# Optimization experiments

Measured on AMD Instinct MI355X. Metric: run time of the kernel, lower is better.

Reference implementation:

```python
import jax, jax.numpy as jnp
import numpy as np

C = 128          # num_channels
S = 3000         # sequence_num
INTER = 30
EXTRACT = S // INTER  # 100
EPS = 1e-5


def _layernorm(y, g, b):
    # LayerNorm over last (channel) axis, eps=1e-5 like torch default
    m = jnp.mean(y, axis=-1, keepdims=True)
    v = jnp.mean(jnp.square(y - m), axis=-1, keepdims=True)
    return (y - m) * jax.lax.rsqrt(v + EPS) * g + b


def setup_inputs() -> dict:
    key = jax.random.key(0)
    ks = jax.random.split(key, 4)
    x = jax.random.normal(ks[0], (32, 4, C, S), dtype=jnp.float32)
    # xavier_normal Linear weights, zero bias; LayerNorm gamma=1, beta=0
    std = float(np.sqrt(2.0 / (C + C)))
    def lin_w(k):
        return jax.random.normal(k, (C, C), dtype=jnp.float32) * std
    Wq = lin_w(ks[1]); Wk = lin_w(ks[2]); Wp = lin_w(ks[3])
    z = jnp.zeros((C,), jnp.float32); o = jnp.ones((C,), jnp.float32)
    return {
        "x": x,
        "Wq": Wq, "bq": z, "gq": o, "betaq": z,
        "Wk": Wk, "bk": z, "gk": o, "betak": z,
        "Wp": Wp, "bp": z, "gp": o, "betap": z,
    }


def reference(x, Wq, bq, gq, betaq, Wk, bk, gk, betak, Wp, bp, gp, betap):
    # x: [b, o, c, s]
    temp = jnp.swapaxes(x, -1, -2)                         # [b,o,s,c]
    q = _layernorm(temp @ Wq.T + bq, gq, betaq)            # [b,o,s,c]
    k = _layernorm(temp @ Wk.T + bk, gk, betak)            # [b,o,s,c]
    q = jnp.swapaxes(q, -1, -2)                            # [b,o,c,s]
    k = jnp.swapaxes(k, -1, -2)                            # [b,o,c,s]
    scaling = jnp.asarray(EXTRACT, x.dtype) ** 0.5         # sqrt(extract_sequence)
    atten = jnp.einsum('bocs,boms->bocm', q, k) / scaling  # [b,o,c,c]
    score = jax.nn.softmax(atten, axis=-1)                 # [b,o,c,c]
    # faithful to source: contracts m (score rows sum to 1)
    out = jnp.einsum('bocs,bocm->bocs', x, score)          # [b,o,c,s]
    out = jnp.swapaxes(out, -1, -2)                        # [b,o,s,c]
    out = _layernorm(out @ Wp.T + bp, gp, betap)
    return jnp.swapaxes(out, -1, -2)                       # [b,o,c,s]
```

## Files before the change

kernel.cpp:

```cpp
#include <hip/hip_runtime.h>


#define C    128
#define SEQ  3000
#define NG   128
#define NT   128
#define NBLK ((SEQ + NT - 1) / NT)

typedef float f4 __attribute__((ext_vector_type(4)));
typedef short short8 __attribute__((ext_vector_type(8)));

__device__ __forceinline__ unsigned short f2bf(float f) {
    union { float f; unsigned u; } v; v.f = f;
    unsigned r = v.u + 0x7fffu + ((v.u >> 16) & 1u);
    return (unsigned short)(r >> 16);
}

__device__ __forceinline__ unsigned cvt2(float lo, float hi) {
    unsigned r;
    asm("v_cvt_pk_bf16_f32 %0, %1, %2" : "=v"(r) : "v"(lo), "v"(hi));
    return r;
}

__device__ __forceinline__ int swz(int row, int chunk) {
    return chunk ^ ((row ^ (row >> 2)) & 15);
}

__global__ void cvt_wp(const float* __restrict__ Wp, unsigned short* __restrict__ out) {
    int i = blockIdx.x * 256 + threadIdx.x;
    if (i >= C * C) return;
    int c = i >> 7, r = i & 127, ch = r >> 3, j = r & 7;
    out[c * C + swz(c, ch) * 8 + j] = f2bf(Wp[i]);
}

__global__ __launch_bounds__(512, 4) void gemm_ln_mfma(
    const float* __restrict__ x,
    const unsigned short* __restrict__ wbf,
    const float* __restrict__ bp,
    const float* __restrict__ gp,
    const float* __restrict__ bep,
    float* __restrict__ out)
{
    __shared__ __align__(16) unsigned short Wl[C * C];
    __shared__ __align__(16) unsigned short Xl[NT * C];

    const int g  = blockIdx.y;
    const int s0 = blockIdx.x * NT;
    const float* xg = x + (size_t)g * (C * SEQ);
    float* og = out + (size_t)g * (C * SEQ);
    const int t = threadIdx.x;

    {
        const uint4* wsrc = (const uint4*)wbf;
        uint4* wdst = (uint4*)Wl;
        #pragma unroll
        for (int i = 0; i < 4; ++i) wdst[t + 512 * i] = wsrc[t + 512 * i];
    }

    {
        const int sq  = t & 31;
        const int mc  = t >> 5;
        const int s_loc  = 4 * sq;
        const int s_glob = s0 + s_loc;
        const bool valid = (s_glob + 3) < SEQ;
        f4 r[8];
        const float* xp = xg + (size_t)(mc * 8) * SEQ + s_glob;
        #pragma unroll
        for (int rr = 0; rr < 8; ++rr) {
            if (valid) r[rr] = *(const f4*)(xp + (size_t)rr * SEQ);
            else       r[rr] = (f4){0.f, 0.f, 0.f, 0.f};
        }
        #pragma unroll
        for (int j = 0; j < 4; ++j) {
            const int sl = s_loc + j;
            uint4 pk;
            pk.x = cvt2(r[0][j], r[1][j]);
            pk.y = cvt2(r[2][j], r[3][j]);
            pk.z = cvt2(r[4][j], r[5][j]);
            pk.w = cvt2(r[6][j], r[7][j]);
            *(uint4*)&Xl[sl * C + swz(sl, mc) * 8] = pk;
        }
    }
    __syncthreads();

    const int w    = t >> 6;
    const int lane = t & 63;
    const int col  = lane & 15;
    const int quad = lane >> 4;

    f4 acc[8];
    #pragma unroll
    for (int mt = 0; mt < 8; ++mt) acc[mt] = (f4){0.f, 0.f, 0.f, 0.f};

    const int srow = 16 * w + col;

    #pragma unroll 1
    for (int kc = 0; kc < 4; ++kc) {
        short8 xb = *(const short8*)&Xl[srow * C + swz(srow, 4 * kc + quad) * 8];
        short8 a[8];
        #pragma unroll
        for (int mt = 0; mt < 8; ++mt) {
            const int row = 16 * mt + col;
            a[mt] = *(const short8*)&Wl[row * C + swz(row, 4 * kc + quad) * 8];
        }
        #pragma unroll
        for (int mt = 0; mt < 8; ++mt)
            acc[mt] = __builtin_amdgcn_mfma_f32_16x16x32_bf16(a[mt], xb, acc[mt], 0, 0, 0);
    }

    #pragma unroll
    for (int mt = 0; mt < 8; ++mt) {
        const f4 b4 = *(const f4*)(bp + 16 * mt + 4 * quad);
        #pragma unroll
        for (int r = 0; r < 4; ++r) acc[mt][r] += b4[r];
    }

    float s = 0.f, q = 0.f;
    #pragma unroll
    for (int mt = 0; mt < 8; ++mt)
        #pragma unroll
        for (int r = 0; r < 4; ++r) {
            float y = acc[mt][r];
            s += y; q += y * y;
        }
    s += __shfl_xor(s, 16); q += __shfl_xor(q, 16);
    s += __shfl_xor(s, 32); q += __shfl_xor(q, 32);
    const float mean = s * (1.0f / C);
    const float var  = q * (1.0f / C) - mean * mean;
    const float rstd = rsqrtf(var + 1e-5f);

    const int sg = s0 + srow;
    if (sg < SEQ) {
        #pragma unroll
        for (int mt = 0; mt < 8; ++mt) {
            const f4 g4 = *(const f4*)(gp  + 16 * mt + 4 * quad);
            const f4 e4 = *(const f4*)(bep + 16 * mt + 4 * quad);
            #pragma unroll
            for (int r = 0; r < 4; ++r) {
                const int c = 16 * mt + 4 * quad + r;
                og[(size_t)c * SEQ + sg] =
                    (acc[mt][r] - mean) * rstd * g4[r] + e4[r];
            }
        }
    }
}

extern "C" void kernel_launch(void* const* d_in, const int* in_sizes, int n_in,
                              void* d_out, int out_size, void* d_ws, size_t ws_size,
                              hipStream_t stream) {
    const float* x   = (const float*)d_in[0];
    const float* Wp  = (const float*)d_in[9];
    const float* bp  = (const float*)d_in[10];
    const float* gp  = (const float*)d_in[11];
    const float* bep = (const float*)d_in[12];
    float* out = (float*)d_out;
    unsigned short* wbf = (unsigned short*)d_ws;

    hipLaunchKernelGGL(cvt_wp, dim3(64), dim3(256), 0, stream, Wp, wbf);

    dim3 grid(NBLK, NG);
    hipLaunchKernelGGL(gemm_ln_mfma, grid, dim3(512), 0, stream,
                       x, wbf, bp, gp, bep, out);
}
```

Baseline: 374.1 us.

## Make GEMM+LayerNorm blocks loop over six sequence tiles with register prefetch

Each block now handles six consecutive 128-column sequence tiles instead of one, so the grid shrinks to 4x128 blocks. The bf16 weight tile is staged into LDS once per block rather than once per tile. The next tile's x values are loaded into registers while the current tile is converted, stored to LDS and run through MFMA and LayerNorm, hiding global-load latency. Out-of-range loads are clamped rather than zero-filled, and explicit s_barrier/lgkmcnt waits replace __syncthreads. The cost is fewer, longer-running blocks, less parallelism across the GPU and more register pressure.

```diff
diff --git a/kernel.cpp b/kernel.cpp
--- a/kernel.cpp
+++ b/kernel.cpp
@@ -5,7 +5,8 @@
 #define SEQ  3000
 #define NG   128
 #define NT   128
-#define NBLK ((SEQ + NT - 1) / NT)
+#define NTILES 6
+#define NBX  4
 
 typedef float f4 __attribute__((ext_vector_type(4)));
 typedef short short8 __attribute__((ext_vector_type(8)));
@@ -24,6 +25,13 @@
 
 __device__ __forceinline__ int swz(int row, int chunk) {
     return chunk ^ ((row ^ (row >> 2)) & 15);
+}
+
+__device__ __forceinline__ void bar_lgkm() {
+    asm volatile("s_waitcnt lgkmcnt(0)\n\ts_barrier" ::: "memory");
+}
+__device__ __forceinline__ void bar_raw() {
+    asm volatile("s_barrier" ::: "memory");
 }
 
 __global__ void cvt_wp(const float* __restrict__ Wp, unsigned short* __restrict__ out) {
@@ -45,7 +53,7 @@
     __shared__ __align__(16) unsigned short Xl[NT * C];
 
     const int g  = blockIdx.y;
-    const int s0 = blockIdx.x * NT;
+    const int bx = blockIdx.x;
     const float* xg = x + (size_t)g * (C * SEQ);
     float* og = out + (size_t)g * (C * SEQ);
     const int t = threadIdx.x;
@@ -57,91 +65,111 @@
         for (int i = 0; i < 4; ++i) wdst[t + 512 * i] = wsrc[t + 512 * i];
     }
 
-    {
-        const int sq  = t & 31;
-        const int mc  = t >> 5;
-        const int s_loc  = 4 * sq;
-        const int s_glob = s0 + s_loc;
-        const bool valid = (s_glob + 3) < SEQ;
-        f4 r[8];
-        const float* xp = xg + (size_t)(mc * 8) * SEQ + s_glob;
-        #pragma unroll
-        for (int rr = 0; rr < 8; ++rr) {
-            if (valid) r[rr] = *(const f4*)(xp + (size_t)rr * SEQ);
-            else       r[rr] = (f4){0.f, 0.f, 0.f, 0.f};
-        }
-        #pragma unroll
-        for (int j = 0; j < 4; ++j) {
-            const int sl = s_loc + j;
-            uint4 pk;
-            pk.x = cvt2(r[0][j], r[1][j]);
-            pk.y = cvt2(r[2][j], r[3][j]);
-            pk.z = cvt2(r[4][j], r[5][j]);
-            pk.w = cvt2(r[6][j], r[7][j]);
-            *(uint4*)&Xl[sl * C + swz(sl, mc) * 8] = pk;
-        }
-    }
-    __syncthreads();
+    const int sq  = t & 31;
+    const int mc  = t >> 5;
+    const int s_loc = 4 * sq;
 
     const int w    = t >> 6;
     const int lane = t & 63;
     const int col  = lane & 15;
     const int quad = lane >> 4;
-
-    f4 acc[8];
-    #pragma unroll
-    for (int mt = 0; mt < 8; ++mt) acc[mt] = (f4){0.f, 0.f, 0.f, 0.f};
-
     const int srow = 16 * w + col;
 
+    const int s_base = bx * (NTILES * NT);
+
+    f4 r[8];
+    {
+        int sgl = s_base + s_loc;
+        int sc  = sgl > (SEQ - 4) ? (SEQ - 4) : sgl;
+        const float* xp = xg + (size_t)(mc * 8) * SEQ + sc;
+        #pragma unroll
+        for (int rr = 0; rr < 8; ++rr) r[rr] = *(const f4*)(xp + (size_t)rr * SEQ);
+    }
+
     #pragma unroll 1
-    for (int kc = 0; kc < 4; ++kc) {
-        short8 xb = *(const short8*)&Xl[srow * C + swz(srow, 4 * kc + quad) * 8];
-        short8 a[8];
+    for (int tt = 0; tt < NTILES; ++tt) {
+        const int s0 = s_base + tt * NT;
+
+        uint4 pk[4];
+        #pragma unroll
+        for (int j = 0; j < 4; ++j) {
+            pk[j].x = cvt2(r[0][j], r[1][j]);
+            pk[j].y = cvt2(r[2][j], r[3][j]);
+            pk[j].z = cvt2(r[4][j], r[5][j]);
+            pk[j].w = cvt2(r[6][j], r[7][j]);
+        }
+
+        if (tt + 1 < NTILES) {
+            int sgl = s0 + NT + s_loc;
+            int sc  = sgl > (SEQ - 4) ? (SEQ - 4) : sgl;
+            const float* xp = xg + (size_t)(mc * 8) * SEQ + sc;
+            #pragma unroll
+            for (int rr = 0; rr < 8; ++rr) r[rr] = *(const f4*)(xp + (size_t)rr * SEQ);
+        }
+
+        #pragma unroll
+        for (int j = 0; j < 4; ++j) {
+            const int sl = s_loc + j;
+            *(uint4*)&Xl[sl * C + swz(sl, mc) * 8] = pk[j];
+        }
+
+        bar_lgkm();
+
+        f4 acc[8];
+        #pragma unroll
+        for (int mt = 0; mt < 8; ++mt) acc[mt] = (f4){0.f, 0.f, 0.f, 0.f};
+
+        #pragma unroll 1
+        for (int kc = 0; kc < 4; ++kc) {
+            short8 xb = *(const short8*)&Xl[srow * C + swz(srow, 4 * kc + quad) * 8];
+            short8 a[8];
+            #pragma unroll
+            for (int mt = 0; mt < 8; ++mt) {
+                const int row = 16 * mt + col;
+                a[mt] = *(const short8*)&Wl[row * C + swz(row, 4 * kc + quad) * 8];
+            }
+            #pragma unroll
+            for (int mt = 0; mt < 8; ++mt)
+                acc[mt] = __builtin_amdgcn_mfma_f32_16x16x32_bf16(a[mt], xb, acc[mt], 0, 0, 0);
+        }
+
         #pragma unroll
         for (int mt = 0; mt < 8; ++mt) {
-            const int row = 16 * mt + col;
-            a[mt] = *(const short8*)&Wl[row * C + swz(row, 4 * kc + quad) * 8];
+            const f4 b4 = *(const f4*)(bp + 16 * mt + 4 * quad);
+            #pragma unroll
+            for (int rr = 0; rr < 4; ++rr) acc[mt][rr] += b4[rr];
         }
+
+        float s = 0.f, q = 0.f;
         #pragma unroll
         for (int mt = 0; mt < 8; ++mt)
-            acc[mt] = __builtin_amdgcn_mfma_f32_16x16x32_bf16(a[mt], xb, acc[mt], 0, 0, 0);
-    }
+            #pragma unroll
+            for (int rr = 0; rr < 4; ++rr) {
+                float y = acc[mt][rr];
+                s += y; q += y * y;
+            }
+        s += __shfl_xor(s, 16); q += __shfl_xor(q, 16);
+        s += __shfl_xor(s, 32); q += __shfl_xor(q, 32);
+        const float mean = s * (1.0f / C);
+        const float var  = q * (1.0f / C) - mean * mean;
+        const float rstd = rsqrtf(var + 1e-5f);
 
-    #pragma unroll
-    for (int mt = 0; mt < 8; ++mt) {
-        const f4 b4 = *(const f4*)(bp + 16 * mt + 4 * quad);
-        #pragma unroll
-        for (int r = 0; r < 4; ++r) acc[mt][r] += b4[r];
-    }
-
-    float s = 0.f, q = 0.f;
-    #pragma unroll
-    for (int mt = 0; mt < 8; ++mt)
-        #pragma unroll
-        for (int r = 0; r < 4; ++r) {
-            float y = acc[mt][r];
-            s += y; q += y * y;
-        }
-    s += __shfl_xor(s, 16); q += __shfl_xor(q, 16);
-    s += __shfl_xor(s, 32); q += __shfl_xor(q, 32);
-    const float mean = s * (1.0f / C);
-    const float var  = q * (1.0f / C) - mean * mean;
-    const float rstd = rsqrtf(var + 1e-5f);
-
-    const int sg = s0 + srow;
-    if (sg < SEQ) {
-        #pragma unroll
-        for (int mt = 0; mt < 8; ++mt) {
-            const f4 g4 = *(const f4*)(gp  + 16 * mt + 4 * quad);
-            const f4 e4 = *(const f4*)(bep + 16 * mt + 4 * quad);
+        const int sg = s0 + srow;
+        if (sg < SEQ) {
             #pragma unroll
-            for (int r = 0; r < 4; ++r) {
-                const int c = 16 * mt + 4 * quad + r;
-                og[(size_t)c * SEQ + sg] =
-                    (acc[mt][r] - mean) * rstd * g4[r] + e4[r];
+            for (int mt = 0; mt < 8; ++mt) {
+                const f4 g4 = *(const f4*)(gp  + 16 * mt + 4 * quad);
+                const f4 e4 = *(const f4*)(bep + 16 * mt + 4 * quad);
+                #pragma unroll
+                for (int rr = 0; rr < 4; ++rr) {
+                    const int c = 16 * mt + 4 * quad + rr;
+                    og[(size_t)c * SEQ + sg] =
+                        (acc[mt][rr] - mean) * rstd * g4[rr] + e4[rr];
+                }
             }
         }
+
+        bar_raw();
     }
 }
 
@@ -158,7 +186,7 @@
 
     hipLaunchKernelGGL(cvt_wp, dim3(64), dim3(256), 0, stream, Wp, wbf);
 
-    dim3 grid(NBLK, NG);
+    dim3 grid(NBX, NG);
     hipLaunchKernelGGL(gemm_ln_mfma, grid, dim3(512), 0, stream,
                        x, wbf, bp, gp, bep, out);
 }
```

Result: slower. 400.0 us (+6.9%).

## Convert GEMM+LayerNorm to persistent waves with register-prefetched 16-row strips

Applied to the files above, without the earlier changes.

Replaces the one-block-per-128-row-tile grid with a persistent grid of 512 blocks. Each wave independently loops over 16-sequence strips, with a per-wave LDS staging buffer. The next strip's x values are prefetched into registers while the current strip runs its MFMA and LayerNorm, so global load latency overlaps compute. The weight LDS fill and the bias, gamma and beta loads are paid once per block instead of once per tile. The cost is higher register pressure and smaller 16-row MFMA tiles per wave, and the last strip clamps its load address rather than zero-filling.

```diff
diff --git a/kernel.cpp b/kernel.cpp
--- a/kernel.cpp
+++ b/kernel.cpp
@@ -4,8 +4,9 @@
 #define C    128
 #define SEQ  3000
 #define NG   128
-#define NT   128
-#define NBLK ((SEQ + NT - 1) / NT)
+#define SPG  188
+#define NSTRIP (NG * SPG)
+#define NWAVE  4096
 
 typedef float f4 __attribute__((ext_vector_type(4)));
 typedef short short8 __attribute__((ext_vector_type(8)));
@@ -42,12 +43,8 @@
     float* __restrict__ out)
 {
     __shared__ __align__(16) unsigned short Wl[C * C];
-    __shared__ __align__(16) unsigned short Xl[NT * C];
+    __shared__ __align__(16) unsigned short Xs[8][16 * C];
 
-    const int g  = blockIdx.y;
-    const int s0 = blockIdx.x * NT;
-    const float* xg = x + (size_t)g * (C * SEQ);
-    float* og = out + (size_t)g * (C * SEQ);
     const int t = threadIdx.x;
 
     {
@@ -56,90 +53,111 @@
         #pragma unroll
         for (int i = 0; i < 4; ++i) wdst[t + 512 * i] = wsrc[t + 512 * i];
     }
-
-    {
-        const int sq  = t & 31;
-        const int mc  = t >> 5;
-        const int s_loc  = 4 * sq;
-        const int s_glob = s0 + s_loc;
-        const bool valid = (s_glob + 3) < SEQ;
-        f4 r[8];
-        const float* xp = xg + (size_t)(mc * 8) * SEQ + s_glob;
-        #pragma unroll
-        for (int rr = 0; rr < 8; ++rr) {
-            if (valid) r[rr] = *(const f4*)(xp + (size_t)rr * SEQ);
-            else       r[rr] = (f4){0.f, 0.f, 0.f, 0.f};
-        }
-        #pragma unroll
-        for (int j = 0; j < 4; ++j) {
-            const int sl = s_loc + j;
-            uint4 pk;
-            pk.x = cvt2(r[0][j], r[1][j]);
-            pk.y = cvt2(r[2][j], r[3][j]);
-            pk.z = cvt2(r[4][j], r[5][j]);
-            pk.w = cvt2(r[6][j], r[7][j]);
-            *(uint4*)&Xl[sl * C + swz(sl, mc) * 8] = pk;
-        }
-    }
     __syncthreads();
 
     const int w    = t >> 6;
     const int lane = t & 63;
     const int col  = lane & 15;
     const int quad = lane >> 4;
+    const int mc   = lane >> 2;
+    const int sq   = lane & 3;
+    unsigned short* X = &Xs[w][0];
 
-    f4 acc[8];
+    const int wgid = blockIdx.x * 8 + w;
+
+    f4 b4[8], g4[8], e4[8];
     #pragma unroll
-    for (int mt = 0; mt < 8; ++mt) acc[mt] = (f4){0.f, 0.f, 0.f, 0.f};
+    for (int mt = 0; mt < 8; ++mt) {
+        b4[mt] = *(const f4*)(bp  + 16 * mt + 4 * quad);
+        g4[mt] = *(const f4*)(gp  + 16 * mt + 4 * quad);
+        e4[mt] = *(const f4*)(bep + 16 * mt + 4 * quad);
+    }
 
-    const int srow = 16 * w + col;
+    f4 r[8];
+    int sid = wgid;
+    if (sid < NSTRIP) {
+        const int g  = sid / SPG;
+        const int s0 = (sid - g * SPG) * 16;
+        int sb = s0 + 4 * sq; if (sb > SEQ - 4) sb = SEQ - 4;
+        const float* xp = x + (size_t)g * (C * SEQ) + (size_t)(mc * 8) * SEQ + sb;
+        #pragma unroll
+        for (int rr = 0; rr < 8; ++rr) r[rr] = *(const f4*)(xp + (size_t)rr * SEQ);
+    }
 
     #pragma unroll 1
-    for (int kc = 0; kc < 4; ++kc) {
-        short8 xb = *(const short8*)&Xl[srow * C + swz(srow, 4 * kc + quad) * 8];
-        short8 a[8];
+    for (; sid < NSTRIP; sid += NWAVE) {
+        const int g  = sid / SPG;
+        const int s0 = (sid - g * SPG) * 16;
+        float* og = out + (size_t)g * (C * SEQ);
+
         #pragma unroll
-        for (int mt = 0; mt < 8; ++mt) {
-            const int row = 16 * mt + col;
-            a[mt] = *(const short8*)&Wl[row * C + swz(row, 4 * kc + quad) * 8];
+        for (int j = 0; j < 4; ++j) {
+            const int sl = 4 * sq + j;
+            uint4 pk;
+            pk.x = cvt2(r[0][j], r[1][j]);
+            pk.y = cvt2(r[2][j], r[3][j]);
+            pk.z = cvt2(r[4][j], r[5][j]);
+            pk.w = cvt2(r[6][j], r[7][j]);
+            *(uint4*)&X[sl * C + swz(sl, mc) * 8] = pk;
         }
+
+        {
+            int nsid = sid + NWAVE; if (nsid >= NSTRIP) nsid = sid;
+            const int ng  = nsid / SPG;
+            const int ns0 = (nsid - ng * SPG) * 16;
+            int sb = ns0 + 4 * sq; if (sb > SEQ - 4) sb = SEQ - 4;
+            const float* xp = x + (size_t)ng * (C * SEQ) + (size_t)(mc * 8) * SEQ + sb;
+            #pragma unroll
+            for (int rr = 0; rr < 8; ++rr) r[rr] = *(const f4*)(xp + (size_t)rr * SEQ);
+        }
+
+        f4 acc[8];
+        #pragma unroll
+        for (int mt = 0; mt < 8; ++mt) acc[mt] = (f4){0.f, 0.f, 0.f, 0.f};
+
+        #pragma unroll 1
+        for (int kc = 0; kc < 4; ++kc) {
+            short8 xb = *(const short8*)&X[col * C + swz(col, 4 * kc + quad) * 8];
+            short8 a[8];
+            #pragma unroll
+            for (int mt = 0; mt < 8; ++mt) {
+                const int row = 16 * mt + col;
+                a[mt] = *(const short8*)&Wl[row * C + swz(row, 4 * kc + quad) * 8];
+            }
+            #pragma unroll
+            for (int mt = 0; mt < 8; ++mt)
+                acc[mt] = __builtin_amdgcn_mfma_f32_16x16x32_bf16(a[mt], xb, acc[mt], 0, 0, 0);
+        }
+
         #pragma unroll
         for (int mt = 0; mt < 8; ++mt)
-            acc[mt] = __builtin_amdgcn_mfma_f32_16x16x32_bf16(a[mt], xb, acc[mt], 0, 0, 0);
-    }
+            #pragma unroll
+            for (int rr = 0; rr < 4; ++rr) acc[mt][rr] += b4[mt][rr];
 
-    #pragma unroll
-    for (int mt = 0; mt < 8; ++mt) {
-        const f4 b4 = *(const f4*)(bp + 16 * mt + 4 * quad);
+        float s = 0.f, q = 0.f;
         #pragma unroll
-        for (int r = 0; r < 4; ++r) acc[mt][r] += b4[r];
-    }
+        for (int mt = 0; mt < 8; ++mt)
+            #pragma unroll
+            for (int rr = 0; rr < 4; ++rr) {
+                float y = acc[mt][rr];
+                s += y; q += y * y;
+            }
+        s += __shfl_xor(s, 16); q += __shfl_xor(q, 16);
+        s += __shfl_xor(s, 32); q += __shfl_xor(q, 32);
+        const float mean = s * (1.0f / C);
+        const float var  = q * (1.0f / C) - mean * mean;
+        const float rstd = rsqrtf(var + 1e-5f);
 
-    float s = 0.f, q = 0.f;
-    #pragma unroll
-    for (int mt = 0; mt < 8; ++mt)
-        #pragma unroll
-        for (int r = 0; r < 4; ++r) {
-            float y = acc[mt][r];
-            s += y; q += y * y;
-        }
-    s += __shfl_xor(s, 16); q += __shfl_xor(q, 16);
-    s += __shfl_xor(s, 32); q += __shfl_xor(q, 32);
-    const float mean = s * (1.0f / C);
-    const float var  = q * (1.0f / C) - mean * mean;
-    const float rstd = rsqrtf(var + 1e-5f);
-
-    const int sg = s0 + srow;
-    if (sg < SEQ) {
-        #pragma unroll
-        for (int mt = 0; mt < 8; ++mt) {
-            const f4 g4 = *(const f4*)(gp  + 16 * mt + 4 * quad);
-            const f4 e4 = *(const f4*)(bep + 16 * mt + 4 * quad);
+        const int sg = s0 + col;
+        if (sg < SEQ) {
             #pragma unroll
-            for (int r = 0; r < 4; ++r) {
-                const int c = 16 * mt + 4 * quad + r;
-                og[(size_t)c * SEQ + sg] =
-                    (acc[mt][r] - mean) * rstd * g4[r] + e4[r];
+            for (int mt = 0; mt < 8; ++mt) {
+                #pragma unroll
+                for (int rr = 0; rr < 4; ++rr) {
+                    const int c = 16 * mt + 4 * quad + rr;
+                    og[(size_t)c * SEQ + sg] =
+                        (acc[mt][rr] - mean) * rstd * g4[mt][rr] + e4[mt][rr];
+                }
             }
         }
     }
@@ -158,7 +176,6 @@
 
     hipLaunchKernelGGL(cvt_wp, dim3(64), dim3(256), 0, stream, Wp, wbf);
 
-    dim3 grid(NBLK, NG);
-    hipLaunchKernelGGL(gemm_ln_mfma, grid, dim3(512), 0, stream,
+    hipLaunchKernelGGL(gemm_ln_mfma, dim3(512), dim3(512), 0, stream,
                        x, wbf, bp, gp, bep, out);
 }
```

Result: slower. 468.7 us (+25.3%).
